# Kernel optimization log

Measured on AMD Instinct MI355X. Metric: run time of the kernel, lower is better.

## Reference

```python
import jax, jax.numpy as jnp
import numpy as np

D = 1024   # feature_dim
K = 10     # num_anchors
B = 16384  # batch
H = 8      # num_heads


def setup_inputs() -> dict:
    key = jax.random.key(0)
    ks = jax.random.split(key, 12)
    f32 = jnp.float32

    def w(k, shape, scale=0.02):
        return (jax.random.normal(k, shape, f32) * scale)

    return {
        "features": jax.random.normal(ks[0], (B, D), f32),
        "anchors": w(ks[1], (K, D), 0.1),
        # anchor_refiner: Linear(D, D//2) -> ReLU -> Linear(D//2, D) -> Tanh
        "ar_w1": w(ks[2], (D, D // 2)), "ar_b1": jnp.zeros((D // 2,), f32),
        "ar_w2": w(ks[3], (D // 2, D)), "ar_b2": jnp.zeros((D,), f32),
        # attention projections
        "q_w": w(ks[4], (D, D)), "q_b": jnp.zeros((D,), f32),
        "k_w": w(ks[5], (D, D)), "k_b": jnp.zeros((D,), f32),
        "v_w": w(ks[6], (D, D)), "v_b": jnp.zeros((D,), f32),
        "o_w": w(ks[7], (D, D)), "o_b": jnp.zeros((D,), f32),
        # feature_enhancer: LayerNorm -> Linear(D,2D) -> GELU -> Linear(2D,D)
        "ln_g": jnp.ones((D,), f32), "ln_b": jnp.zeros((D,), f32),
        "ff_w1": w(ks[8], (D, 2 * D)), "ff_b1": jnp.zeros((2 * D,), f32),
        "ff_w2": w(ks[9], (2 * D, D)), "ff_b2": jnp.zeros((D,), f32),
        "div_w": jnp.asarray(0.001, f32),
        "cen_w": jnp.asarray(0.001, f32),
    }


def _l2norm(x, eps=1e-8):
    n = jnp.linalg.norm(x, axis=-1, keepdims=True)
    return x / jnp.maximum(n, eps)


def _layernorm(x, g, b, eps=1e-5):
    mu = jnp.mean(x, axis=-1, keepdims=True)
    var = jnp.mean(jnp.square(x - mu), axis=-1, keepdims=True)
    return (x - mu) * jax.lax.rsqrt(var + eps) * g + b


def reference(features, anchors, ar_w1, ar_b1, ar_w2, ar_b2,
              q_w, q_b, k_w, k_b, v_w, v_b, o_w, o_b,
              ln_g, ln_b, ff_w1, ff_b1, ff_w2, ff_b2, div_w, cen_w):
    b = features.shape[0]
    hd = D // H
    fn = _l2norm(features)                                 # [B, D]

    # anchor refinement
    refin = jnp.tanh(jax.nn.relu(anchors @ ar_w1 + ar_b1) @ ar_w2 + ar_b2)
    an = _l2norm(anchors + 0.1 * refin)                    # [K, D]

    # multi-head cross-attention to anchors
    q = (fn @ q_w + q_b).reshape(b, H, hd)                 # [B, H, hd]
    k = (an @ k_w + k_b).reshape(K, H, hd)                 # [K, H, hd]
    v = (an @ v_w + v_b).reshape(K, H, hd)
    scores = jnp.einsum('bhd,khd->bhk', q, k) / jnp.sqrt(jnp.asarray(hd, fn.dtype))
    aw = jax.nn.softmax(scores, axis=-1)                   # [B, H, K]
    att = jnp.einsum('bhk,khd->bhd', aw, v).reshape(b, D)
    att = att @ o_w + o_b

    # feature enhancer (dropout inactive: eval mode)
    enh = fn + 0.1 * att
    h = jax.nn.gelu(_layernorm(enh, ln_g, ln_b) @ ff_w1 + ff_b1, approximate=False)
    enh = h @ ff_w2 + ff_b2
    final = fn + 0.2 * enh                                 # [B, D]

    # diversity loss: pdist over K=10 anchors (45 pairs)
    diff = an[:, None, :] - an[None, :, :]                 # [K, K, D]
    dmat = jnp.sqrt(jnp.maximum(jnp.sum(diff * diff, -1), 1e-24))
    iu = np.triu_indices(K, 1)
    div_loss = jnp.exp(-jnp.maximum(dmat[iu].mean(), 1e-6))

    # center loss: attention-weighted feature-anchor distances
    avg_att = aw.mean(axis=1)                              # [B, K]
    sq = (jnp.sum(fn * fn, 1, keepdims=True) + jnp.sum(an * an, 1)
          - 2.0 * fn @ an.T)
    fa_dist = jnp.sqrt(jnp.maximum(sq, 1e-12))             # [B, K]
    center_loss = jnp.sum(avg_att * fa_dist, axis=1).mean()

    geo = jnp.abs(div_w) * div_loss + jnp.abs(cen_w) * center_loss
    geo = jnp.clip(geo, 0.0, 0.01)
    return final, geo
```

## Files before the change

### kernel.cpp

```cpp
#include <hip/hip_runtime.h>
#include <hip/hip_bf16.h>
#include <math.h>

typedef __hip_bfloat16 bf16;

#define D_  1024
#define K_  10
#define B_  16384
#define H_  8
#define HD_ 128

struct alignas(16) BF8 { bf16 v[8]; };
struct alignas(8)  BF4 { bf16 v[4]; };

typedef __bf16 bf8v __attribute__((ext_vector_type(8)));
typedef float  f4v  __attribute__((ext_vector_type(4)));

__device__ __forceinline__ float b2f(bf16 x){ return __bfloat162float(x); }
__device__ __forceinline__ bf16  f2b(float x){ return __float2bfloat16(x); }

#define GL2LDS16(g, l) __builtin_amdgcn_global_load_lds( \
    (__attribute__((address_space(1))) void*)(g), \
    (__attribute__((address_space(3))) void*)(l), 16, 0, 0)

__global__ __launch_bounds__(256) void l2norm_k(const float* __restrict__ x,
                                                bf16* __restrict__ fnb) {
  int b = blockIdx.x, t = threadIdx.x;
  float4 v = ((const float4*)(x + (size_t)b * D_))[t];
  float p = v.x*v.x + v.y*v.y + v.z*v.z + v.w*v.w;
  #pragma unroll
  for (int o = 32; o > 0; o >>= 1) p += __shfl_down(p, o);
  __shared__ float wsum[4];
  if ((t & 63) == 0) wsum[t >> 6] = p;
  __syncthreads();
  __shared__ float inv_s;
  if (t == 0) inv_s = 1.f / fmaxf(sqrtf(wsum[0]+wsum[1]+wsum[2]+wsum[3]), 1e-8f);
  __syncthreads();
  float iv = inv_s;
  BF4 o;
  o.v[0] = f2b(v.x*iv); o.v[1] = f2b(v.y*iv);
  o.v[2] = f2b(v.z*iv); o.v[3] = f2b(v.w*iv);
  ((BF4*)(fnb + (size_t)b * D_))[t] = o;
}

__global__ __launch_bounds__(256) void wt3_k(
    const float* __restrict__ qw, const float* __restrict__ w1,
    const float* __restrict__ w2,
    bf16* __restrict__ o_qw, bf16* __restrict__ o_w1, bf16* __restrict__ o_w2) {
  __shared__ float tle[32][33];
  int b = blockIdx.x;
  const float* w; bf16* wt; int R, C, c0, r0;
  if (b < 1024)      { w = qw; wt = o_qw; R = 1024; C = 1024;
                       c0 = (b & 31) * 32;      r0 = (b >> 5) * 32; }
  else if (b < 3072) { int i = b - 1024; w = w1; wt = o_w1; R = 1024; C = 2048;
                       c0 = (i % 64) * 32;      r0 = (i / 64) * 32; }
  else               { int i = b - 3072; w = w2; wt = o_w2; R = 2048; C = 1024;
                       c0 = (i % 32) * 32;      r0 = (i / 32) * 32; }
  int tx = threadIdx.x & 31, ty = threadIdx.x >> 5;
  #pragma unroll
  for (int i = 0; i < 32; i += 8)
    tle[ty + i][tx] = w[(size_t)(r0 + ty + i) * C + c0 + tx];
  __syncthreads();
  #pragma unroll
  for (int i = 0; i < 32; i += 8)
    wt[(size_t)(c0 + ty + i) * R + r0 + tx] = f2b(tle[tx][ty + i]);
}

template<int COLS, int KD, int ACT>
__global__ __launch_bounds__(256) void panelmm_k(
    const float* __restrict__ A, const float* __restrict__ W,
    const float* __restrict__ bias, const float* __restrict__ aux,
    float* __restrict__ out,
    const float* __restrict__ W2, const float* __restrict__ bias2,
    float* __restrict__ out2, int N, int npanel) {
  constexpr int GROUPS = 256 / COLS;
  constexpr int DCH = KD / GROUPS;
  __shared__ float A_s[K_][KD];
  __shared__ float part[K_][COLS][GROUPS];
  const int t = threadIdx.x;
  int blk = blockIdx.x;
  const float* Wm = W; const float* bm = bias; float* om = out;
  if (blk >= npanel) { blk -= npanel; Wm = W2; bm = bias2; om = out2; }
  const int panel = blk;
  for (int i = t; i < K_*KD; i += 256) A_s[0][i] = A[i];
  __syncthreads();
  const int cg = t % COLS, g = t / COLS;
  const int col = panel*COLS + cg;
  float s[K_];
  #pragma unroll
  for (int r = 0; r < K_; ++r) s[r] = 0.f;
  const float* wp = Wm + (size_t)(g*DCH)*N + col;
  for (int d = g*DCH; d < (g+1)*DCH; ++d) {
    float wv = *wp; wp += N;
    #pragma unroll
    for (int r = 0; r < K_; ++r) s[r] = fmaf(A_s[r][d], wv, s[r]);
  }
  #pragma unroll
  for (int r = 0; r < K_; ++r) part[r][cg][g] = s[r];
  __syncthreads();
  for (int o = t; o < K_*COLS; o += 256) {
    int r = o / COLS, c = o % COLS;
    float v = 0.f;
    #pragma unroll
    for (int gg = 0; gg < GROUPS; ++gg) v += part[r][c][gg];
    v += bm[panel*COLS + c];
    if constexpr (ACT == 1) v = fmaxf(v, 0.f);
    if constexpr (ACT == 2) v = aux[(size_t)r*N + panel*COLS + c] + 0.1f*tanhf(v);
    om[(size_t)r*N + panel*COLS + c] = v;
  }
}

__global__ __launch_bounds__(256) void ar3_k(const float* __restrict__ an_un,
    float* __restrict__ an, float* __restrict__ na, float* __restrict__ divloss) {
  __shared__ float a_s[K_][D_];
  __shared__ float nrm[K_];
  __shared__ float dm[45];
  const int t = threadIdx.x;
  for (int i = t; i < K_*D_; i += 256) a_s[0][i] = an_un[i];
  __syncthreads();
  const int wid = t >> 6, lane = t & 63;
  for (int r = wid; r < K_; r += 4) {
    float p = 0.f;
    for (int j = lane; j < D_; j += 64) p += a_s[r][j]*a_s[r][j];
    #pragma unroll
    for (int o = 1; o < 64; o <<= 1) p += __shfl_xor(p, o);
    if (lane == 0) nrm[r] = p;
  }
  __syncthreads();
  for (int i = t; i < K_*D_; i += 256) {
    int r = i >> 10;
    float iv = 1.f / fmaxf(sqrtf(nrm[r]), 1e-8f);
    float v = a_s[0][i] * iv;
    a_s[0][i] = v;
    an[i] = v;
  }
  if (t < K_) {
    float iv = 1.f / fmaxf(sqrtf(nrm[t]), 1e-8f);
    na[t] = nrm[t] * iv * iv;
  }
  __syncthreads();
  const int pr = t >> 2, sub = t & 3;
  if (pr < 45) {
    int i = 0, j = 0, c = pr;
    for (i = 0; i < K_; ++i) { int cnt = K_-1-i; if (c < cnt) { j = i+1+c; break; } c -= cnt; }
    float s = 0.f;
    for (int d = sub*256; d < sub*256 + 256; ++d) {
      float df = a_s[i][d] - a_s[j][d]; s += df*df;
    }
    s += __shfl_xor(s, 1); s += __shfl_xor(s, 2);
    if (sub == 0) dm[pr] = sqrtf(fmaxf(s, 1e-24f));
  }
  __syncthreads();
  if (t == 0) {
    float m = 0.f;
    for (int p = 0; p < 45; ++p) m += dm[p];
    m *= (1.f/45.f);
    *divloss = expf(-fmaxf(m, 1e-6f));
  }
}

template<int TRANSOUT, typename TW>
__device__ __forceinline__ void smallmm_body(
    int blk, const float* __restrict__ A, const TW* __restrict__ W,
    bf16* __restrict__ outb, float scale,
    float (&A_s)[K_][128], float (&part)[K_][64][4]) {
  constexpr int COLS = 64, GROUPS = 4, DCH = 32, NW = 1024;
  const int t = threadIdx.x;
  const int h = blk & 7, panel = blk >> 3;
  for (int i = t; i < K_*128; i += 256) {
    int r = i >> 7, j = i & 127;
    A_s[r][j] = A[r*1024 + h*128 + j];
  }
  __syncthreads();
  const int cg = t % COLS, g = t / COLS;
  const int col = panel*COLS + cg;
  float s[K_];
  #pragma unroll
  for (int r = 0; r < K_; ++r) s[r] = 0.f;
  const TW* wp = W + (size_t)(h*128 + g*DCH)*NW + col;
  for (int d = 0; d < DCH; ++d) {
    float wv;
    if constexpr (sizeof(TW) == 2) wv = b2f(*wp); else wv = *wp;
    wp += NW;
    #pragma unroll
    for (int r = 0; r < K_; ++r) s[r] = fmaf(A_s[r][g*DCH + d], wv, s[r]);
  }
  #pragma unroll
  for (int r = 0; r < K_; ++r) part[r][cg][g] = s[r];
  __syncthreads();
  for (int o = t; o < 16*COLS; o += 256) {
    int r = o / COLS, c = o % COLS;
    float v = 0.f;
    if (r < K_) {
      #pragma unroll
      for (int gg = 0; gg < GROUPS; ++gg) v += part[r][c][gg];
      v *= scale;
    }
    if constexpr (TRANSOUT) outb[(size_t)(panel*COLS + c)*128 + h*16 + r] = f2b(v);
    else                    outb[(size_t)(h*16 + r)*NW + panel*COLS + c] = f2b(v);
  }
}

__global__ __launch_bounds__(256) void prep_k(
    const float* __restrict__ Km, const float* __restrict__ Vm,
    const float* __restrict__ an, const float* __restrict__ na,
    const bf16* __restrict__ wq, const float* __restrict__ ow,
    const float* __restrict__ qb,
    bf16* __restrict__ wt, bf16* __restrict__ vt, float* __restrict__ sb) {
  __shared__ float A_s[K_][128];
  __shared__ float part[K_][64][4];
  const int b = blockIdx.x;
  if (b < 128) {
    smallmm_body<0, bf16>(b, Km, wq, wt, 0.08838834764831845f, A_s, part);
  } else if (b < 256) {
    smallmm_body<1, float>(b - 128, Vm, ow, vt, 1.f, A_s, part);
  } else if (b < 384) {
    int k = b - 256;
    bf16* dst = wt + (size_t)(128 + k) * 1024;
    int i = threadIdx.x * 4;
    BF4 o;
    if (k < K_) {
      float4 a = *(const float4*)(an + (size_t)k*1024 + i);
      o.v[0] = f2b(-2.f*a.x); o.v[1] = f2b(-2.f*a.y);
      o.v[2] = f2b(-2.f*a.z); o.v[3] = f2b(-2.f*a.w);
    } else {
      o.v[0] = o.v[1] = o.v[2] = o.v[3] = f2b(0.f);
    }
    *(BF4*)(dst + i) = o;
  } else {
    int c = threadIdx.x;
    if (c < 128) {
      int h = c >> 4, k = c & 15;
      float s = 0.f;
      if (k < K_) {
        for (int j = 0; j < HD_; ++j)
          s = fmaf(qb[h*HD_ + j], Km[(size_t)k*D_ + h*HD_ + j], s);
      }
      sb[c] = s * 0.08838834764831845f;
    } else {
      int j = c - 128;
      sb[c] = (j < K_) ? (1.f + na[j]) : 0.f;
    }
  }
}

template<int EPI, int KD, typename TO>
__global__ __launch_bounds__(256) void mgemm_k(
    const bf16* __restrict__ A, const bf16* __restrict__ Bt,
    const float* __restrict__ bias, const bf16* __restrict__ aux,
    TO* __restrict__ out, int M, int N, float scale) {
  constexpr int BM = 128, BN = 128, BK = 32;
  constexpr int nt = KD / BK;
  __shared__ bf16 As[2][BM*BK];
  __shared__ bf16 Bs[2][BN*BK];
  const int tid = threadIdx.x;
  const int nMB = M / BM;
  const int nwg = gridDim.x;
  int wg = blockIdx.x;
  wg = (wg & 7) * (nwg >> 3) + (wg >> 3);
  const int bm = (wg % nMB) * BM, bn = (wg / nMB) * BN;

  const int srow = tid >> 2;
  const int ssw  = (((tid & 3) ^ ((tid >> 3) & 3)) * 8);
  const bf16* gA = A  + (size_t)(bm + srow) * KD + ssw;
  const bf16* gB = Bt + (size_t)(bn + srow) * KD + ssw;
  const size_t rstep = (size_t)64 * KD;

  const int w    = tid >> 6;
  const int lane = tid & 63;
  const int wr = (w >> 1) * 64, wc = (w & 1) * 64;
  const int fr = lane & 15, fg = lane >> 4;
  const int key = (fr >> 1) & 3;
  const int co  = (fg ^ key) * 8;

  f4v acc[4][4];
  const f4v zz = {0.f, 0.f, 0.f, 0.f};
  #pragma unroll
  for (int m = 0; m < 4; ++m)
    #pragma unroll
    for (int n = 0; n < 4; ++n) acc[m][n] = zz;

  GL2LDS16(gA,         &As[0][0] + tid*8);
  GL2LDS16(gA + rstep, &As[0][0] + tid*8 + 2048);
  GL2LDS16(gB,         &Bs[0][0] + tid*8);
  GL2LDS16(gB + rstep, &Bs[0][0] + tid*8 + 2048);
  __syncthreads();

  #pragma unroll 2
  for (int t = 0; t < nt; ++t) {
    const int buf = t & 1;
    if (t + 1 < nt) {
      const int ko = (t + 1) * BK;
      GL2LDS16(gA + ko,         &As[buf^1][0] + tid*8);
      GL2LDS16(gA + rstep + ko, &As[buf^1][0] + tid*8 + 2048);
      GL2LDS16(gB + ko,         &Bs[buf^1][0] + tid*8);
      GL2LDS16(gB + rstep + ko, &Bs[buf^1][0] + tid*8 + 2048);
    }
    const bf16* la = &As[buf][0];
    const bf16* lb = &Bs[buf][0];
    bf8v af[4], bq[4];
    #pragma unroll
    for (int m = 0; m < 4; ++m)
      af[m] = *(const bf8v*)(la + (wr + m*16 + fr)*BK + co);
    #pragma unroll
    for (int n = 0; n < 4; ++n)
      bq[n] = *(const bf8v*)(lb + (wc + n*16 + fr)*BK + co);
    __builtin_amdgcn_s_setprio(1);
    #pragma unroll
    for (int m = 0; m < 4; ++m)
      #pragma unroll
      for (int n = 0; n < 4; ++n)
        acc[m][n] = __builtin_amdgcn_mfma_f32_16x16x32_bf16(af[m], bq[n], acc[m][n], 0, 0, 0);
    __builtin_amdgcn_s_setprio(0);
    __syncthreads();
  }

  float bv[4];
  #pragma unroll
  for (int n = 0; n < 4; ++n) bv[n] = bias[bn + wc + n*16 + fr];
  #pragma unroll
  for (int m = 0; m < 4; ++m) {
    #pragma unroll
    for (int r = 0; r < 4; ++r) {
      const int row = bm + wr + m*16 + fg*4 + r;
      #pragma unroll
      for (int n = 0; n < 4; ++n) {
        const int col = bn + wc + n*16 + fr;
        float x = acc[m][n][r] + bv[n];
        if constexpr (EPI == 1) x = b2f(aux[(size_t)row * N + col]) + scale * x;
        if constexpr (EPI == 2) x = 0.5f * x * (1.f + erff(x * 0.70710678118654752f));
        if constexpr (sizeof(TO) == 2) out[(size_t)row * N + col] = f2b(x);
        else                           out[(size_t)row * N + col] = x;
      }
    }
  }
}

template<int EPI, int KD, typename TO>
__global__ __launch_bounds__(512) void mgemm256_k(
    const bf16* __restrict__ A, const bf16* __restrict__ Bt,
    const float* __restrict__ bias, const bf16* __restrict__ aux,
    TO* __restrict__ out, int M, int N, float scale) {
  constexpr int BM = 256, BN = 256, BK = 64;
  constexpr int nt = KD / BK;
  __shared__ bf16 As[2][BM*BK];
  __shared__ bf16 Bs[2][BN*BK];
  const int tid = threadIdx.x;
  const int nMB = M / BM;
  const int nwg = gridDim.x;
  int wg = blockIdx.x;
  wg = (wg & 7) * (nwg >> 3) + (wg >> 3);
  const int bm = (wg % nMB) * BM, bn = (wg / nMB) * BN;

  const int srow = tid >> 3;
  const int scsw = ((tid & 7) ^ (srow & 7)) * 8;
  const bf16* gA = A  + (size_t)(bm + srow) * KD + scsw;
  const bf16* gB = Bt + (size_t)(bn + srow) * KD + scsw;
  const size_t lstep = (size_t)64 * KD;

  const int wid = tid >> 6, lane = tid & 63;
  const int wm = wid >> 2, wn = wid & 3;
  const int fr = lane & 15, fg = lane >> 4;
  const int fsw = fr & 7;
  const int c0 = ((fg     ^ fsw) * 8);
  const int c1 = (((4+fg) ^ fsw) * 8);

  f4v acc[8][4];
  const f4v zz = {0.f, 0.f, 0.f, 0.f};
  #pragma unroll
  for (int m = 0; m < 8; ++m)
    #pragma unroll
    for (int n = 0; n < 4; ++n) acc[m][n] = zz;

  #pragma unroll
  for (int l = 0; l < 4; ++l) {
    GL2LDS16(gA + l*lstep, &As[0][0] + tid*8 + l*4096);
    GL2LDS16(gB + l*lstep, &Bs[0][0] + tid*8 + l*4096);
  }
  __syncthreads();

  #pragma unroll 2
  for (int t = 0; t < nt; ++t) {
    const int buf = t & 1;
    if (t + 1 < nt) {
      const int ko = (t + 1) * BK;
      #pragma unroll
      for (int l = 0; l < 4; ++l) {
        GL2LDS16(gA + l*lstep + ko, &As[buf^1][0] + tid*8 + l*4096);
        GL2LDS16(gB + l*lstep + ko, &Bs[buf^1][0] + tid*8 + l*4096);
      }
    }
    const bf16* la = &As[buf][0];
    const bf16* lb = &Bs[buf][0];
    bf8v bq[8];
    #pragma unroll
    for (int n = 0; n < 4; ++n) {
      const int rb = wn*64 + n*16 + fr;
      bq[n*2]   = *(const bf8v*)(lb + rb*64 + c0);
      bq[n*2+1] = *(const bf8v*)(lb + rb*64 + c1);
    }
    __builtin_amdgcn_s_setprio(1);
    #pragma unroll
    for (int m = 0; m < 8; ++m) {
      const int ra = wm*128 + m*16 + fr;
      bf8v a0 = *(const bf8v*)(la + ra*64 + c0);
      bf8v a1 = *(const bf8v*)(la + ra*64 + c1);
      #pragma unroll
      for (int n = 0; n < 4; ++n) {
        acc[m][n] = __builtin_amdgcn_mfma_f32_16x16x32_bf16(a0, bq[n*2],   acc[m][n], 0, 0, 0);
        acc[m][n] = __builtin_amdgcn_mfma_f32_16x16x32_bf16(a1, bq[n*2+1], acc[m][n], 0, 0, 0);
      }
    }
    __builtin_amdgcn_s_setprio(0);
    __syncthreads();
  }

  float bv[4];
  #pragma unroll
  for (int n = 0; n < 4; ++n) bv[n] = bias[bn + wn*64 + n*16 + fr];
  #pragma unroll
  for (int m = 0; m < 8; ++m) {
    #pragma unroll
    for (int r = 0; r < 4; ++r) {
      const int row = bm + wm*128 + m*16 + fg*4 + r;
      #pragma unroll
      for (int n = 0; n < 4; ++n) {
        const int col = bn + wn*64 + n*16 + fr;
        float x = acc[m][n][r] + bv[n];
        if constexpr (EPI == 1) x = b2f(aux[(size_t)row * N + col]) + scale * x;
        if constexpr (EPI == 2) x = 0.5f * x * (1.f + erff(x * 0.70710678118654752f));
        if constexpr (sizeof(TO) == 2) out[(size_t)row * N + col] = f2b(x);
        else                           out[(size_t)row * N + col] = x;
      }
    }
  }
}

__global__ __launch_bounds__(256) void attn2_k(
    const float* __restrict__ S, bf16* __restrict__ awp,
    float* __restrict__ cen_acc) {
  __shared__ float cred[4];
  const int t = threadIdx.x;
  const int wid = t >> 6, lane = t & 63;
  const int sub = lane & 7, head = lane >> 3;
  const int k0 = sub*2, k1 = k0 + 1;
  float c_acc = 0.f;
  const int row0 = blockIdx.x * 32 + wid * 8;

  for (int i = 0; i < 8; ++i) {
    const int row = row0 + i;
    const float* Sr = S + (size_t)row * 256;
    float2 sv = *(const float2*)(Sr + head*16 + k0);
    float v0 = (k0 < K_) ? sv.x : -1e30f;
    float v1 = (k1 < K_) ? sv.y : -1e30f;
    float m = fmaxf(v0, v1);
    m = fmaxf(m, __shfl_xor(m,1)); m = fmaxf(m, __shfl_xor(m,2)); m = fmaxf(m, __shfl_xor(m,4));
    float e0 = (k0 < K_) ? __expf(v0 - m) : 0.f;
    float e1 = (k1 < K_) ? __expf(v1 - m) : 0.f;
    float es = e0 + e1;
    es += __shfl_xor(es,1); es += __shfl_xor(es,2); es += __shfl_xor(es,4);
    float inv = 1.f / es;
    float a0 = e0 * inv, a1 = e1 * inv;
    bf16 b0 = f2b(a0), b1 = f2b(a1);
    unsigned int pk = (unsigned int)(*(unsigned short*)&b0)
                    | ((unsigned int)(*(unsigned short*)&b1) << 16);
    *(unsigned int*)(awp + (size_t)row*128 + head*16 + k0) = pk;
    float g0 = a0, g1 = a1;
    g0 += __shfl_xor(g0,8); g0 += __shfl_xor(g0,16); g0 += __shfl_xor(g0,32);
    g1 += __shfl_xor(g1,8); g1 += __shfl_xor(g1,16); g1 += __shfl_xor(g1,32);
    if (sub < 5) {
      float d20 = Sr[128 + k0];
      float d21 = Sr[128 + k1];
      c_acc = fmaf(g0, sqrtf(fmaxf(d20, 1e-12f)), c_acc);
      c_acc = fmaf(g1, sqrtf(fmaxf(d21, 1e-12f)), c_acc);
    }
  }
  #pragma unroll
  for (int o = 1; o < 64; o <<= 1) c_acc += __shfl_xor(c_acc, o);
  if (lane == 0) cred[wid] = c_acc;
  __syncthreads();
  if (t == 0) {
    float s = (cred[0]+cred[1]+cred[2]+cred[3]) * (1.f/64.f/(float)B_);
    atomicAdd(cen_acc, s);
  }
}

__global__ __launch_bounds__(256) void ln_k(const bf16* __restrict__ x,
    const float* __restrict__ g, const float* __restrict__ bta,
    bf16* __restrict__ out) {
  int b = blockIdx.x, t = threadIdx.x;
  BF4 ld = ((const BF4*)(x + (size_t)b * D_))[t];
  float v[4];
  #pragma unroll
  for (int j = 0; j < 4; ++j) v[j] = b2f(ld.v[j]);
  float s = v[0]+v[1]+v[2]+v[3];
  #pragma unroll
  for (int o = 32; o > 0; o >>= 1) s += __shfl_down(s, o);
  __shared__ float w1[4], w2[4];
  if ((t & 63) == 0) w1[t >> 6] = s;
  __syncthreads();
  __shared__ float mu_s, rs_s;
  if (t == 0) mu_s = (w1[0]+w1[1]+w1[2]+w1[3]) * (1.f/D_);
  __syncthreads();
  float mu = mu_s;
  float qv = 0.f;
  #pragma unroll
  for (int j = 0; j < 4; ++j) { float d = v[j]-mu; qv += d*d; }
  #pragma unroll
  for (int o = 32; o > 0; o >>= 1) qv += __shfl_down(qv, o);
  if ((t & 63) == 0) w2[t >> 6] = qv;
  __syncthreads();
  if (t == 0) rs_s = rsqrtf((w2[0]+w2[1]+w2[2]+w2[3]) * (1.f/D_) + 1e-5f);
  __syncthreads();
  float rs = rs_s;
  BF4 o;
  #pragma unroll
  for (int j = 0; j < 4; ++j) {
    int col = t*4 + j;
    o.v[j] = f2b((v[j]-mu)*rs*g[col] + bta[col]);
  }
  ((BF4*)(out + (size_t)b * D_))[t] = o;
}

__global__ void geo_k(const float* __restrict__ divl, const float* __restrict__ cen,
                      const float* __restrict__ div_w, const float* __restrict__ cen_w,
                      float* __restrict__ out) {
  float g = fabsf(*div_w) * (*divl) + fabsf(*cen_w) * (*cen);
  out[0] = fminf(fmaxf(g, 0.f), 0.01f);
}

extern "C" void kernel_launch(void* const* d_in, const int* in_sizes, int n_in,
                              void* d_out, int out_size, void* d_ws, size_t ws_size,
                              hipStream_t stream) {
  const float* features = (const float*)d_in[0];
  const float* anchors  = (const float*)d_in[1];
  const float* ar_w1 = (const float*)d_in[2];
  const float* ar_b1 = (const float*)d_in[3];
  const float* ar_w2 = (const float*)d_in[4];
  const float* ar_b2 = (const float*)d_in[5];
  const float* q_w = (const float*)d_in[6];
  const float* q_b = (const float*)d_in[7];
  const float* k_w = (const float*)d_in[8];
  const float* k_b = (const float*)d_in[9];
  const float* v_w = (const float*)d_in[10];
  const float* v_b = (const float*)d_in[11];
  const float* o_w = (const float*)d_in[12];
  const float* o_b = (const float*)d_in[13];
  const float* ln_g = (const float*)d_in[14];
  const float* ln_b = (const float*)d_in[15];
  const float* ff_w1 = (const float*)d_in[16];
  const float* ff_b1 = (const float*)d_in[17];
  const float* ff_w2 = (const float*)d_in[18];
  const float* ff_b2 = (const float*)d_in[19];
  const float* div_w = (const float*)d_in[20];
  const float* cen_w = (const float*)d_in[21];
  float* out = (float*)d_out;

  char* w = (char*)d_ws;
  bf16* ws_fnb = (bf16*)w;  w += (size_t)B_ * D_ * 2;
  bf16* ws_enh = (bf16*)w;  w += (size_t)B_ * D_ * 2;
  bf16* ws_ln  = (bf16*)w;  w += (size_t)B_ * D_ * 2;
  bf16* ws_h   = (bf16*)w;  w += (size_t)B_ * 2048 * 2;
  float* ws_S  = (float*)w; w += (size_t)B_ * 256 * 4;
  bf16* ws_awp = (bf16*)w;  w += (size_t)B_ * 128 * 2;
  bf16* ws_wq  = (bf16*)w;  w += (size_t)D_ * D_ * 2;
  bf16* ws_w1t = (bf16*)w;  w += (size_t)D_ * 2048 * 2;
  bf16* ws_w2t = (bf16*)w;  w += (size_t)2048 * D_ * 2;
  bf16* ws_wt  = (bf16*)w;  w += (size_t)256 * D_ * 2;
  bf16* ws_vt  = (bf16*)w;  w += (size_t)D_ * 128 * 2;
  float* ws_har = (float*)w;  w += (size_t)K_ * (D_/2) * 4;
  float* ws_anu = (float*)w;  w += (size_t)K_ * D_ * 4;
  float* ws_an  = (float*)w;  w += (size_t)K_ * D_ * 4;
  float* ws_k   = (float*)w;  w += (size_t)K_ * D_ * 4;
  float* ws_v   = (float*)w;  w += (size_t)K_ * D_ * 4;
  float* ws_na  = (float*)w;  w += 256;
  float* ws_div = (float*)w;  w += 256;
  float* ws_cen = (float*)w;  w += 256;
  float* ws_sb  = (float*)w;  w += 512;
  if ((size_t)(w - (char*)d_ws) > ws_size) return;

  hipMemsetAsync(ws_cen, 0, 4, stream);

  wt3_k<<<5120, 256, 0, stream>>>(q_w, ff_w1, ff_w2, ws_wq, ws_w1t, ws_w2t);

  l2norm_k<<<B_, 256, 0, stream>>>(features, ws_fnb);

  panelmm_k<32, 1024, 1><<<16, 256, 0, stream>>>(
      anchors, ar_w1, ar_b1, nullptr, ws_har,
      nullptr, nullptr, nullptr, D_/2, 16);
  panelmm_k<64, 512, 2><<<16, 256, 0, stream>>>(
      ws_har, ar_w2, ar_b2, anchors, ws_anu,
      nullptr, nullptr, nullptr, D_, 16);
  ar3_k<<<1, 256, 0, stream>>>(ws_anu, ws_an, ws_na, ws_div);
  panelmm_k<64, 1024, 0><<<32, 256, 0, stream>>>(
      ws_an, k_w, k_b, nullptr, ws_k,
      v_w, v_b, ws_v, D_, 16);

  prep_k<<<385, 256, 0, stream>>>(ws_k, ws_v, ws_an, ws_na,
                                  ws_wq, o_w, q_b, ws_wt, ws_vt, ws_sb);

  mgemm_k<0, 1024, float><<<dim3((B_/128)*(256/128)), 256, 0, stream>>>(
      ws_fnb, ws_wt, ws_sb, nullptr, ws_S, B_, 256, 0.f);

  attn2_k<<<B_/32, 256, 0, stream>>>(ws_S, ws_awp, ws_cen);

  mgemm_k<1, 128, bf16><<<dim3((B_/128)*(D_/128)), 256, 0, stream>>>(
      ws_awp, ws_vt, o_b, ws_fnb, ws_enh, B_, D_, 0.1f);

  ln_k<<<B_, 256, 0, stream>>>(ws_enh, ln_g, ln_b, ws_ln);

  mgemm256_k<2, 1024, bf16><<<dim3((B_/256)*(2048/256)), 512, 0, stream>>>(
      ws_ln, ws_w1t, ff_b1, nullptr, ws_h, B_, 2048, 0.f);

  mgemm256_k<1, 2048, float><<<dim3((B_/256)*(D_/256)), 512, 0, stream>>>(
      ws_h, ws_w2t, ff_b2, ws_fnb, out, B_, D_, 0.2f);

  geo_k<<<1, 1, 0, stream>>>(ws_div, ws_cen, div_w, cen_w, out + (size_t)B_ * D_);
}
```

Measured before the change: 399.7 us.

## Fuse small anchor-path kernels into large elementwise launches and merge K/V into prep

Merges the weight-transpose kernel with the first anchor-refiner matmul, and the feature L2-norm kernel with the second refiner matmul. Each pair becomes one launch whose extra blocks handle the small matmul. The separate K/V projection kernel is folded into the prep kernel: every prep block recomputes its head slice of K or V from the normalized anchors, then applies the q_w / o_w contraction. The aim is fewer kernel launches and inter-kernel bubbles on the serial anchor path. The cost is redundant K/V recomputation across the 16 column panels and a long 1024-deep serial loop per thread in prep blocks, which may lengthen that stage.

```diff
diff --git a/kernel.cpp b/kernel.cpp
--- a/kernel.cpp
+++ b/kernel.cpp
@@ -23,90 +23,115 @@
     (__attribute__((address_space(1))) void*)(g), \
     (__attribute__((address_space(3))) void*)(l), 16, 0, 0)
 
-__global__ __launch_bounds__(256) void l2norm_k(const float* __restrict__ x,
-                                                bf16* __restrict__ fnb) {
-  int b = blockIdx.x, t = threadIdx.x;
-  float4 v = ((const float4*)(x + (size_t)b * D_))[t];
-  float p = v.x*v.x + v.y*v.y + v.z*v.z + v.w*v.w;
-  #pragma unroll
-  for (int o = 32; o > 0; o >>= 1) p += __shfl_down(p, o);
-  __shared__ float wsum[4];
-  if ((t & 63) == 0) wsum[t >> 6] = p;
-  __syncthreads();
-  __shared__ float inv_s;
-  if (t == 0) inv_s = 1.f / fmaxf(sqrtf(wsum[0]+wsum[1]+wsum[2]+wsum[3]), 1e-8f);
-  __syncthreads();
-  float iv = inv_s;
-  BF4 o;
-  o.v[0] = f2b(v.x*iv); o.v[1] = f2b(v.y*iv);
-  o.v[2] = f2b(v.z*iv); o.v[3] = f2b(v.w*iv);
-  ((BF4*)(fnb + (size_t)b * D_))[t] = o;
-}
-
-__global__ __launch_bounds__(256) void wt3_k(
+__global__ __launch_bounds__(256) void mega1_k(
     const float* __restrict__ qw, const float* __restrict__ w1,
     const float* __restrict__ w2,
-    bf16* __restrict__ o_qw, bf16* __restrict__ o_w1, bf16* __restrict__ o_w2) {
-  __shared__ float tle[32][33];
-  int b = blockIdx.x;
-  const float* w; bf16* wt; int R, C, c0, r0;
-  if (b < 1024)      { w = qw; wt = o_qw; R = 1024; C = 1024;
-                       c0 = (b & 31) * 32;      r0 = (b >> 5) * 32; }
-  else if (b < 3072) { int i = b - 1024; w = w1; wt = o_w1; R = 1024; C = 2048;
-                       c0 = (i % 64) * 32;      r0 = (i / 64) * 32; }
-  else               { int i = b - 3072; w = w2; wt = o_w2; R = 2048; C = 1024;
-                       c0 = (i % 32) * 32;      r0 = (i / 32) * 32; }
-  int tx = threadIdx.x & 31, ty = threadIdx.x >> 5;
-  #pragma unroll
-  for (int i = 0; i < 32; i += 8)
-    tle[ty + i][tx] = w[(size_t)(r0 + ty + i) * C + c0 + tx];
-  __syncthreads();
-  #pragma unroll
-  for (int i = 0; i < 32; i += 8)
-    wt[(size_t)(c0 + ty + i) * R + r0 + tx] = f2b(tle[tx][ty + i]);
-}
-
-template<int COLS, int KD, int ACT>
-__global__ __launch_bounds__(256) void panelmm_k(
-    const float* __restrict__ A, const float* __restrict__ W,
-    const float* __restrict__ bias, const float* __restrict__ aux,
-    float* __restrict__ out,
-    const float* __restrict__ W2, const float* __restrict__ bias2,
-    float* __restrict__ out2, int N, int npanel) {
-  constexpr int GROUPS = 256 / COLS;
-  constexpr int DCH = KD / GROUPS;
-  __shared__ float A_s[K_][KD];
-  __shared__ float part[K_][COLS][GROUPS];
+    bf16* __restrict__ o_qw, bf16* __restrict__ o_w1, bf16* __restrict__ o_w2,
+    const float* __restrict__ anchors, const float* __restrict__ ar_w1,
+    const float* __restrict__ ar_b1, float* __restrict__ har) {
+  __shared__ char smem[51200];
+  const int b = blockIdx.x;
   const int t = threadIdx.x;
-  int blk = blockIdx.x;
-  const float* Wm = W; const float* bm = bias; float* om = out;
-  if (blk >= npanel) { blk -= npanel; Wm = W2; bm = bias2; om = out2; }
-  const int panel = blk;
-  for (int i = t; i < K_*KD; i += 256) A_s[0][i] = A[i];
-  __syncthreads();
-  const int cg = t % COLS, g = t / COLS;
-  const int col = panel*COLS + cg;
-  float s[K_];
-  #pragma unroll
-  for (int r = 0; r < K_; ++r) s[r] = 0.f;
-  const float* wp = Wm + (size_t)(g*DCH)*N + col;
-  for (int d = g*DCH; d < (g+1)*DCH; ++d) {
-    float wv = *wp; wp += N;
-    #pragma unroll
-    for (int r = 0; r < K_; ++r) s[r] = fmaf(A_s[r][d], wv, s[r]);
-  }
-  #pragma unroll
-  for (int r = 0; r < K_; ++r) part[r][cg][g] = s[r];
-  __syncthreads();
-  for (int o = t; o < K_*COLS; o += 256) {
-    int r = o / COLS, c = o % COLS;
-    float v = 0.f;
-    #pragma unroll
-    for (int gg = 0; gg < GROUPS; ++gg) v += part[r][c][gg];
-    v += bm[panel*COLS + c];
-    if constexpr (ACT == 1) v = fmaxf(v, 0.f);
-    if constexpr (ACT == 2) v = aux[(size_t)r*N + panel*COLS + c] + 0.1f*tanhf(v);
-    om[(size_t)r*N + panel*COLS + c] = v;
+  if (b < 5120) {
+    float (*tle)[33] = (float(*)[33])smem;
+    const float* w; bf16* wt; int R, C, c0, r0;
+    if (b < 1024)      { w = qw; wt = o_qw; R = 1024; C = 1024;
+                         c0 = (b & 31) * 32;      r0 = (b >> 5) * 32; }
+    else if (b < 3072) { int i = b - 1024; w = w1; wt = o_w1; R = 1024; C = 2048;
+                         c0 = (i % 64) * 32;      r0 = (i / 64) * 32; }
+    else               { int i = b - 3072; w = w2; wt = o_w2; R = 2048; C = 1024;
+                         c0 = (i % 32) * 32;      r0 = (i / 32) * 32; }
+    int tx = t & 31, ty = t >> 5;
+    #pragma unroll
+    for (int i = 0; i < 32; i += 8)
+      tle[ty + i][tx] = w[(size_t)(r0 + ty + i) * C + c0 + tx];
+    __syncthreads();
+    #pragma unroll
+    for (int i = 0; i < 32; i += 8)
+      wt[(size_t)(c0 + ty + i) * R + r0 + tx] = f2b(tle[tx][ty + i]);
+  } else {
+    float (*A_s)[1024]  = (float(*)[1024])smem;
+    float (*part)[32][8] = (float(*)[32][8])(smem + 40960);
+    const int panel = b - 5120;
+    for (int i = t; i < K_*1024; i += 256) A_s[0][i] = anchors[i];
+    __syncthreads();
+    const int cg = t & 31, g = t >> 5;
+    const int col = panel*32 + cg;
+    float s[K_];
+    #pragma unroll
+    for (int r = 0; r < K_; ++r) s[r] = 0.f;
+    const float* wp = ar_w1 + (size_t)(g*128)*512 + col;
+    for (int d = g*128; d < g*128 + 128; ++d) {
+      float wv = *wp; wp += 512;
+      #pragma unroll
+      for (int r = 0; r < K_; ++r) s[r] = fmaf(A_s[r][d], wv, s[r]);
+    }
+    #pragma unroll
+    for (int r = 0; r < K_; ++r) part[r][cg][g] = s[r];
+    __syncthreads();
+    for (int o = t; o < K_*32; o += 256) {
+      int r = o >> 5, c = o & 31;
+      float v = 0.f;
+      #pragma unroll
+      for (int gg = 0; gg < 8; ++gg) v += part[r][c][gg];
+      v += ar_b1[panel*32 + c];
+      har[(size_t)r*512 + panel*32 + c] = fmaxf(v, 0.f);
+    }
+  }
+}
+
+__global__ __launch_bounds__(256) void mega2_k(
+    const float* __restrict__ x, bf16* __restrict__ fnb,
+    const float* __restrict__ har, const float* __restrict__ ar_w2,
+    const float* __restrict__ ar_b2, const float* __restrict__ anchors,
+    float* __restrict__ anu) {
+  __shared__ char smem[30720];
+  const int b = blockIdx.x;
+  const int t = threadIdx.x;
+  if (b < 16384) {
+    float* wsum = (float*)smem;
+    float4 v = ((const float4*)(x + (size_t)b * D_))[t];
+    float p = v.x*v.x + v.y*v.y + v.z*v.z + v.w*v.w;
+    #pragma unroll
+    for (int o = 32; o > 0; o >>= 1) p += __shfl_down(p, o);
+    if ((t & 63) == 0) wsum[t >> 6] = p;
+    __syncthreads();
+    if (t == 0) wsum[4] = 1.f / fmaxf(sqrtf(wsum[0]+wsum[1]+wsum[2]+wsum[3]), 1e-8f);
+    __syncthreads();
+    float iv = wsum[4];
+    BF4 o;
+    o.v[0] = f2b(v.x*iv); o.v[1] = f2b(v.y*iv);
+    o.v[2] = f2b(v.z*iv); o.v[3] = f2b(v.w*iv);
+    ((BF4*)(fnb + (size_t)b * D_))[t] = o;
+  } else {
+    float (*A_s)[512]   = (float(*)[512])smem;
+    float (*part)[64][4] = (float(*)[64][4])(smem + 20480);
+    const int panel = b - 16384;
+    for (int i = t; i < K_*512; i += 256) A_s[0][i] = har[i];
+    __syncthreads();
+    const int cg = t & 63, g = t >> 6;
+    const int col = panel*64 + cg;
+    float s[K_];
+    #pragma unroll
+    for (int r = 0; r < K_; ++r) s[r] = 0.f;
+    const float* wp = ar_w2 + (size_t)(g*128)*1024 + col;
+    for (int d = g*128; d < g*128 + 128; ++d) {
+      float wv = *wp; wp += 1024;
+      #pragma unroll
+      for (int r = 0; r < K_; ++r) s[r] = fmaf(A_s[r][d], wv, s[r]);
+    }
+    #pragma unroll
+    for (int r = 0; r < K_; ++r) part[r][cg][g] = s[r];
+    __syncthreads();
+    for (int o = t; o < K_*64; o += 256) {
+      int r = o >> 6, c = o & 63;
+      float v = 0.f;
+      #pragma unroll
+      for (int gg = 0; gg < 4; ++gg) v += part[r][c][gg];
+      v += ar_b2[panel*64 + c];
+      anu[(size_t)r*1024 + panel*64 + c] =
+          anchors[(size_t)r*1024 + panel*64 + c] + 0.1f*tanhf(v);
+    }
   }
 }
 
@@ -159,65 +184,83 @@
   }
 }
 
-template<int TRANSOUT, typename TW>
-__device__ __forceinline__ void smallmm_body(
-    int blk, const float* __restrict__ A, const TW* __restrict__ W,
-    bf16* __restrict__ outb, float scale,
-    float (&A_s)[K_][128], float (&part)[K_][64][4]) {
-  constexpr int COLS = 64, GROUPS = 4, DCH = 32, NW = 1024;
-  const int t = threadIdx.x;
-  const int h = blk & 7, panel = blk >> 3;
-  for (int i = t; i < K_*128; i += 256) {
-    int r = i >> 7, j = i & 127;
-    A_s[r][j] = A[r*1024 + h*128 + j];
-  }
-  __syncthreads();
-  const int cg = t % COLS, g = t / COLS;
-  const int col = panel*COLS + cg;
-  float s[K_];
-  #pragma unroll
-  for (int r = 0; r < K_; ++r) s[r] = 0.f;
-  const TW* wp = W + (size_t)(h*128 + g*DCH)*NW + col;
-  for (int d = 0; d < DCH; ++d) {
-    float wv;
-    if constexpr (sizeof(TW) == 2) wv = b2f(*wp); else wv = *wp;
-    wp += NW;
-    #pragma unroll
-    for (int r = 0; r < K_; ++r) s[r] = fmaf(A_s[r][g*DCH + d], wv, s[r]);
-  }
-  #pragma unroll
-  for (int r = 0; r < K_; ++r) part[r][cg][g] = s[r];
-  __syncthreads();
-  for (int o = t; o < 16*COLS; o += 256) {
-    int r = o / COLS, c = o % COLS;
-    float v = 0.f;
-    if (r < K_) {
-      #pragma unroll
-      for (int gg = 0; gg < GROUPS; ++gg) v += part[r][c][gg];
-      v *= scale;
-    }
-    if constexpr (TRANSOUT) outb[(size_t)(panel*COLS + c)*128 + h*16 + r] = f2b(v);
-    else                    outb[(size_t)(h*16 + r)*NW + panel*COLS + c] = f2b(v);
-  }
-}
-
-__global__ __launch_bounds__(256) void prep_k(
-    const float* __restrict__ Km, const float* __restrict__ Vm,
+__global__ __launch_bounds__(256) void prep2_k(
     const float* __restrict__ an, const float* __restrict__ na,
+    const float* __restrict__ k_w, const float* __restrict__ k_b,
+    const float* __restrict__ v_w, const float* __restrict__ v_b,
     const bf16* __restrict__ wq, const float* __restrict__ ow,
     const float* __restrict__ qb,
     bf16* __restrict__ wt, bf16* __restrict__ vt, float* __restrict__ sb) {
-  __shared__ float A_s[K_][128];
-  __shared__ float part[K_][64][4];
+  __shared__ char smem[56320];
   const int b = blockIdx.x;
-  if (b < 128) {
-    smallmm_body<0, bf16>(b, Km, wq, wt, 0.08838834764831845f, A_s, part);
-  } else if (b < 256) {
-    smallmm_body<1, float>(b - 128, Vm, ow, vt, 1.f, A_s, part);
-  } else if (b < 384) {
-    int k = b - 256;
+  const int t = threadIdx.x;
+  if (b < 256) {
+    const bool isK = b < 128;
+    const int h = b & 7, p = (b & 127) >> 3;
+    float (*an_s)[1024] = (float(*)[1024])smem;
+    float (*KV_s)[128]  = (float(*)[128])(smem + 40960);
+    float (*part)[64][4] = (float(*)[64][4])(smem + 46080);
+    const float* w_in = isK ? k_w : v_w;
+    const float* b_in = isK ? k_b : v_b;
+    for (int i = t; i < K_*1024; i += 256) an_s[0][i] = an[i];
+    __syncthreads();
+    #pragma unroll
+    for (int it = 0; it < 5; ++it) {
+      const int idx = it*256 + t;
+      const int k = idx >> 7, j = idx & 127;
+      float s = b_in[h*128 + j];
+      const float* wp = w_in + h*128 + j;
+      for (int d = 0; d < 1024; ++d) { s = fmaf(an_s[k][d], wp[0], s); wp += 1024; }
+      KV_s[k][j] = s;
+    }
+    __syncthreads();
+    if (isK && p == 0 && t < 16) {
+      float s = 0.f;
+      if (t < K_) {
+        for (int j = 0; j < 128; ++j) s = fmaf(qb[h*128 + j], KV_s[t][j], s);
+        s *= 0.08838834764831845f;
+      }
+      sb[h*16 + t] = s;
+    }
+    const int cg = t & 63, g = t >> 6;
+    const int col = p*64 + cg;
+    float s[K_];
+    #pragma unroll
+    for (int r = 0; r < K_; ++r) s[r] = 0.f;
+    if (isK) {
+      const bf16* wp = wq + (size_t)(h*128 + g*32)*1024 + col;
+      for (int d = 0; d < 32; ++d) {
+        float wv = b2f(*wp); wp += 1024;
+        #pragma unroll
+        for (int r = 0; r < K_; ++r) s[r] = fmaf(KV_s[r][g*32 + d], wv, s[r]);
+      }
+    } else {
+      const float* wp = ow + (size_t)(h*128 + g*32)*1024 + col;
+      for (int d = 0; d < 32; ++d) {
+        float wv = *wp; wp += 1024;
+        #pragma unroll
+        for (int r = 0; r < K_; ++r) s[r] = fmaf(KV_s[r][g*32 + d], wv, s[r]);
+      }
+    }
+    #pragma unroll
+    for (int r = 0; r < K_; ++r) part[r][cg][g] = s[r];
+    __syncthreads();
+    const float scale = isK ? 0.08838834764831845f : 1.f;
+    for (int o = t; o < 16*64; o += 256) {
+      int r = o >> 6, c = o & 63;
+      float v = 0.f;
+      if (r < K_) {
+        #pragma unroll
+        for (int gg = 0; gg < 4; ++gg) v += part[r][c][gg];
+        v *= scale;
+      }
+      if (isK) wt[(size_t)(h*16 + r)*1024 + p*64 + c] = f2b(v);
+      else     vt[(size_t)(p*64 + c)*128 + h*16 + r]  = f2b(v);
+    }
+  } else {
+    const int k = b - 256;
     bf16* dst = wt + (size_t)(128 + k) * 1024;
-    int i = threadIdx.x * 4;
+    int i = t * 4;
     BF4 o;
     if (k < K_) {
       float4 a = *(const float4*)(an + (size_t)k*1024 + i);
@@ -227,20 +270,7 @@
       o.v[0] = o.v[1] = o.v[2] = o.v[3] = f2b(0.f);
     }
     *(BF4*)(dst + i) = o;
-  } else {
-    int c = threadIdx.x;
-    if (c < 128) {
-      int h = c >> 4, k = c & 15;
-      float s = 0.f;
-      if (k < K_) {
-        for (int j = 0; j < HD_; ++j)
-          s = fmaf(qb[h*HD_ + j], Km[(size_t)k*D_ + h*HD_ + j], s);
-      }
-      sb[c] = s * 0.08838834764831845f;
-    } else {
-      int j = c - 128;
-      sb[c] = (j < K_) ? (1.f + na[j]) : 0.f;
-    }
+    if (k == 0 && t < 16) sb[128 + t] = (t < K_) ? (1.f + na[t]) : 0.f;
   }
 }
 
@@ -571,8 +601,6 @@
   float* ws_har = (float*)w;  w += (size_t)K_ * (D_/2) * 4;
   float* ws_anu = (float*)w;  w += (size_t)K_ * D_ * 4;
   float* ws_an  = (float*)w;  w += (size_t)K_ * D_ * 4;
-  float* ws_k   = (float*)w;  w += (size_t)K_ * D_ * 4;
-  float* ws_v   = (float*)w;  w += (size_t)K_ * D_ * 4;
   float* ws_na  = (float*)w;  w += 256;
   float* ws_div = (float*)w;  w += 256;
   float* ws_cen = (float*)w;  w += 256;
@@ -581,23 +609,14 @@
 
   hipMemsetAsync(ws_cen, 0, 4, stream);
 
-  wt3_k<<<5120, 256, 0, stream>>>(q_w, ff_w1, ff_w2, ws_wq, ws_w1t, ws_w2t);
-
-  l2norm_k<<<B_, 256, 0, stream>>>(features, ws_fnb);
-
-  panelmm_k<32, 1024, 1><<<16, 256, 0, stream>>>(
-      anchors, ar_w1, ar_b1, nullptr, ws_har,
-      nullptr, nullptr, nullptr, D_/2, 16);
-  panelmm_k<64, 512, 2><<<16, 256, 0, stream>>>(
-      ws_har, ar_w2, ar_b2, anchors, ws_anu,
-      nullptr, nullptr, nullptr, D_, 16);
+  mega1_k<<<5136, 256, 0, stream>>>(q_w, ff_w1, ff_w2, ws_wq, ws_w1t, ws_w2t,
+                                    anchors, ar_w1, ar_b1, ws_har);
+  mega2_k<<<16400, 256, 0, stream>>>(features, ws_fnb, ws_har, ar_w2, ar_b2,
+                                     anchors, ws_anu);
   ar3_k<<<1, 256, 0, stream>>>(ws_anu, ws_an, ws_na, ws_div);
-  panelmm_k<64, 1024, 0><<<32, 256, 0, stream>>>(
-      ws_an, k_w, k_b, nullptr, ws_k,
-      v_w, v_b, ws_v, D_, 16);
-
-  prep_k<<<385, 256, 0, stream>>>(ws_k, ws_v, ws_an, ws_na,
-                                  ws_wq, o_w, q_b, ws_wt, ws_vt, ws_sb);
+
+  prep2_k<<<384, 256, 0, stream>>>(ws_an, ws_na, k_w, k_b, v_w, v_b,
+                                   ws_wq, o_w, q_b, ws_wt, ws_vt, ws_sb);
 
   mgemm_k<0, 1024, float><<<dim3((B_/128)*(256/128)), 256, 0, stream>>>(
       ws_fnb, ws_wt, ws_sb, nullptr, ws_S, B_, 256, 0.f);
```

New measurement: 469.3 us. 1.17x slower.

## Merge anchor refiner matmuls into weight-transpose and l2norm kernels

Applied to the files above, without the earlier changes.

Replaces four launches (weight transpose, feature l2norm, two anchor-refiner panel matmuls) with two heterogeneous kernels. Extra blocks appended to the transpose and l2norm grids compute the refiner layers. This removes launch gaps and lets the small serial refiner work overlap with the large bandwidth-bound kernels. In exchange, every block now reserves the large shared-memory footprint the panel blocks need, which can lower occupancy of the memory-bound transpose and normalization blocks.

```diff
diff --git a/kernel.cpp b/kernel.cpp
--- a/kernel.cpp
+++ b/kernel.cpp
@@ -23,47 +23,116 @@
     (__attribute__((address_space(1))) void*)(g), \
     (__attribute__((address_space(3))) void*)(l), 16, 0, 0)
 
-__global__ __launch_bounds__(256) void l2norm_k(const float* __restrict__ x,
-                                                bf16* __restrict__ fnb) {
-  int b = blockIdx.x, t = threadIdx.x;
-  float4 v = ((const float4*)(x + (size_t)b * D_))[t];
-  float p = v.x*v.x + v.y*v.y + v.z*v.z + v.w*v.w;
-  #pragma unroll
-  for (int o = 32; o > 0; o >>= 1) p += __shfl_down(p, o);
-  __shared__ float wsum[4];
-  if ((t & 63) == 0) wsum[t >> 6] = p;
-  __syncthreads();
-  __shared__ float inv_s;
-  if (t == 0) inv_s = 1.f / fmaxf(sqrtf(wsum[0]+wsum[1]+wsum[2]+wsum[3]), 1e-8f);
-  __syncthreads();
-  float iv = inv_s;
-  BF4 o;
-  o.v[0] = f2b(v.x*iv); o.v[1] = f2b(v.y*iv);
-  o.v[2] = f2b(v.z*iv); o.v[3] = f2b(v.w*iv);
-  ((BF4*)(fnb + (size_t)b * D_))[t] = o;
-}
-
-__global__ __launch_bounds__(256) void wt3_k(
+__global__ __launch_bounds__(256) void mega1_k(
     const float* __restrict__ qw, const float* __restrict__ w1,
     const float* __restrict__ w2,
-    bf16* __restrict__ o_qw, bf16* __restrict__ o_w1, bf16* __restrict__ o_w2) {
-  __shared__ float tle[32][33];
-  int b = blockIdx.x;
-  const float* w; bf16* wt; int R, C, c0, r0;
-  if (b < 1024)      { w = qw; wt = o_qw; R = 1024; C = 1024;
-                       c0 = (b & 31) * 32;      r0 = (b >> 5) * 32; }
-  else if (b < 3072) { int i = b - 1024; w = w1; wt = o_w1; R = 1024; C = 2048;
-                       c0 = (i % 64) * 32;      r0 = (i / 64) * 32; }
-  else               { int i = b - 3072; w = w2; wt = o_w2; R = 2048; C = 1024;
-                       c0 = (i % 32) * 32;      r0 = (i / 32) * 32; }
-  int tx = threadIdx.x & 31, ty = threadIdx.x >> 5;
-  #pragma unroll
-  for (int i = 0; i < 32; i += 8)
-    tle[ty + i][tx] = w[(size_t)(r0 + ty + i) * C + c0 + tx];
-  __syncthreads();
-  #pragma unroll
-  for (int i = 0; i < 32; i += 8)
-    wt[(size_t)(c0 + ty + i) * R + r0 + tx] = f2b(tle[tx][ty + i]);
+    bf16* __restrict__ o_qw, bf16* __restrict__ o_w1, bf16* __restrict__ o_w2,
+    const float* __restrict__ anchors, const float* __restrict__ ar_w1,
+    const float* __restrict__ ar_b1, float* __restrict__ har) {
+  __shared__ char smem[51200];
+  const int b = blockIdx.x;
+  const int t = threadIdx.x;
+  if (b < 5120) {
+    float (*tle)[33] = (float(*)[33])smem;
+    const float* w; bf16* wt; int R, C, c0, r0;
+    if (b < 1024)      { w = qw; wt = o_qw; R = 1024; C = 1024;
+                         c0 = (b & 31) * 32;      r0 = (b >> 5) * 32; }
+    else if (b < 3072) { int i = b - 1024; w = w1; wt = o_w1; R = 1024; C = 2048;
+                         c0 = (i % 64) * 32;      r0 = (i / 64) * 32; }
+    else               { int i = b - 3072; w = w2; wt = o_w2; R = 2048; C = 1024;
+                         c0 = (i % 32) * 32;      r0 = (i / 32) * 32; }
+    int tx = t & 31, ty = t >> 5;
+    #pragma unroll
+    for (int i = 0; i < 32; i += 8)
+      tle[ty + i][tx] = w[(size_t)(r0 + ty + i) * C + c0 + tx];
+    __syncthreads();
+    #pragma unroll
+    for (int i = 0; i < 32; i += 8)
+      wt[(size_t)(c0 + ty + i) * R + r0 + tx] = f2b(tle[tx][ty + i]);
+  } else {
+    float (*A_s)[1024]  = (float(*)[1024])smem;
+    float (*part)[32][8] = (float(*)[32][8])(smem + 40960);
+    const int panel = b - 5120;
+    for (int i = t; i < K_*1024; i += 256) A_s[0][i] = anchors[i];
+    __syncthreads();
+    const int cg = t & 31, g = t >> 5;
+    const int col = panel*32 + cg;
+    float s[K_];
+    #pragma unroll
+    for (int r = 0; r < K_; ++r) s[r] = 0.f;
+    const float* wp = ar_w1 + (size_t)(g*128)*512 + col;
+    for (int d = g*128; d < g*128 + 128; ++d) {
+      float wv = *wp; wp += 512;
+      #pragma unroll
+      for (int r = 0; r < K_; ++r) s[r] = fmaf(A_s[r][d], wv, s[r]);
+    }
+    #pragma unroll
+    for (int r = 0; r < K_; ++r) part[r][cg][g] = s[r];
+    __syncthreads();
+    for (int o = t; o < K_*32; o += 256) {
+      int r = o >> 5, c = o & 31;
+      float v = 0.f;
+      #pragma unroll
+      for (int gg = 0; gg < 8; ++gg) v += part[r][c][gg];
+      v += ar_b1[panel*32 + c];
+      har[(size_t)r*512 + panel*32 + c] = fmaxf(v, 0.f);
+    }
+  }
+}
+
+__global__ __launch_bounds__(256) void mega2_k(
+    const float* __restrict__ x, bf16* __restrict__ fnb,
+    const float* __restrict__ har, const float* __restrict__ ar_w2,
+    const float* __restrict__ ar_b2, const float* __restrict__ anchors,
+    float* __restrict__ anu) {
+  __shared__ char smem[30720];
+  const int b = blockIdx.x;
+  const int t = threadIdx.x;
+  if (b < 16384) {
+    float* wsum = (float*)smem;
+    float4 v = ((const float4*)(x + (size_t)b * D_))[t];
+    float p = v.x*v.x + v.y*v.y + v.z*v.z + v.w*v.w;
+    #pragma unroll
+    for (int o = 32; o > 0; o >>= 1) p += __shfl_down(p, o);
+    if ((t & 63) == 0) wsum[t >> 6] = p;
+    __syncthreads();
+    if (t == 0) wsum[4] = 1.f / fmaxf(sqrtf(wsum[0]+wsum[1]+wsum[2]+wsum[3]), 1e-8f);
+    __syncthreads();
+    float iv = wsum[4];
+    BF4 o;
+    o.v[0] = f2b(v.x*iv); o.v[1] = f2b(v.y*iv);
+    o.v[2] = f2b(v.z*iv); o.v[3] = f2b(v.w*iv);
+    ((BF4*)(fnb + (size_t)b * D_))[t] = o;
+  } else {
+    float (*A_s)[512]   = (float(*)[512])smem;
+    float (*part)[64][4] = (float(*)[64][4])(smem + 20480);
+    const int panel = b - 16384;
+    for (int i = t; i < K_*512; i += 256) A_s[0][i] = har[i];
+    __syncthreads();
+    const int cg = t & 63, g = t >> 6;
+    const int col = panel*64 + cg;
+    float s[K_];
+    #pragma unroll
+    for (int r = 0; r < K_; ++r) s[r] = 0.f;
+    const float* wp = ar_w2 + (size_t)(g*128)*1024 + col;
+    for (int d = g*128; d < g*128 + 128; ++d) {
+      float wv = *wp; wp += 1024;
+      #pragma unroll
+      for (int r = 0; r < K_; ++r) s[r] = fmaf(A_s[r][d], wv, s[r]);
+    }
+    #pragma unroll
+    for (int r = 0; r < K_; ++r) part[r][cg][g] = s[r];
+    __syncthreads();
+    for (int o = t; o < K_*64; o += 256) {
+      int r = o >> 6, c = o & 63;
+      float v = 0.f;
+      #pragma unroll
+      for (int gg = 0; gg < 4; ++gg) v += part[r][c][gg];
+      v += ar_b2[panel*64 + c];
+      anu[(size_t)r*1024 + panel*64 + c] =
+          anchors[(size_t)r*1024 + panel*64 + c] + 0.1f*tanhf(v);
+    }
+  }
 }
 
 template<int COLS, int KD, int ACT>
@@ -581,17 +650,12 @@
 
   hipMemsetAsync(ws_cen, 0, 4, stream);
 
-  wt3_k<<<5120, 256, 0, stream>>>(q_w, ff_w1, ff_w2, ws_wq, ws_w1t, ws_w2t);
-
-  l2norm_k<<<B_, 256, 0, stream>>>(features, ws_fnb);
-
-  panelmm_k<32, 1024, 1><<<16, 256, 0, stream>>>(
-      anchors, ar_w1, ar_b1, nullptr, ws_har,
-      nullptr, nullptr, nullptr, D_/2, 16);
-  panelmm_k<64, 512, 2><<<16, 256, 0, stream>>>(
-      ws_har, ar_w2, ar_b2, anchors, ws_anu,
-      nullptr, nullptr, nullptr, D_, 16);
+  mega1_k<<<5136, 256, 0, stream>>>(q_w, ff_w1, ff_w2, ws_wq, ws_w1t, ws_w2t,
+                                    anchors, ar_w1, ar_b1, ws_har);
+  mega2_k<<<16400, 256, 0, stream>>>(features, ws_fnb, ws_har, ar_w2, ar_b2,
+                                     anchors, ws_anu);
   ar3_k<<<1, 256, 0, stream>>>(ws_anu, ws_an, ws_na, ws_div);
+
   panelmm_k<64, 1024, 0><<<32, 256, 0, stream>>>(
       ws_an, k_w, k_b, nullptr, ws_k,
       v_w, v_b, ws_v, D_, 16);
```

Result: no change. 401.7 us, median of 2 (+0.5%).
